# Performance work log

Hardware: AMD Instinct MI355X
Metric: run time of the kernel (lower is better)

Reference implementation:

```python
import jax, jax.numpy as jnp
import numpy as np

MARGIN = 200.0
EPS = 1e-6  # torch F.pairwise_distance default eps (added to the difference)


def setup_inputs() -> dict:
    key = jax.random.key(0)
    k1, k2, k3 = jax.random.split(key, 3)
    B2, T, D = 128, 1024, 1024  # 2*batch_size, snippets, feature dim
    scores = jax.random.normal(k1, (B2, T), dtype=jnp.float32)
    feats = jax.random.normal(k2, (B2, T, D), dtype=jnp.float32)
    targets = jax.random.uniform(k3, (B2, T), dtype=jnp.float32)
    return {"scores": scores, "feats": feats, "targets": targets}


def _bce_with_logits(logits, targets):
    # mean over all elements of max(x,0) - x*t + log(1+exp(-|x|))
    return jnp.mean(jnp.maximum(logits, 0.0) - logits * targets
                    + jnp.log1p(jnp.exp(-jnp.abs(logits))))


def _contrastive(M):
    # M: [2b, T] feature magnitudes (L1 norms). Split into normal / abnormal.
    b = M.shape[0] // 2
    n_f, a_f = M[:b], M[b:]
    # pairwise euclidean distance d_ij = ||n_i - a_j + eps||_2   [b, b]
    diff = n_f[:, None, :] - a_f[None, :, :] + EPS
    dist = jnp.sqrt(jnp.sum(diff * diff, axis=-1))
    d = jnp.square(jnp.maximum(MARGIN - dist, 0.0))
    # strict '<' in the torch loop => first flat occurrence of the min
    flat_idx = jnp.argmin(d.reshape(-1))
    i_star = flat_idx // b
    j_star = flat_idx % b
    min_d = d.reshape(-1)[flat_idx]
    loss_con = 0.001 * min_d
    # loss_n: sum_{i != i*} ||n_i - n_{i*} + eps||^2 / b
    dn = n_f - n_f[i_star] + EPS
    sq_n = jnp.sum(dn * dn, axis=-1)          # [b]
    loss_n = (jnp.sum(sq_n) - sq_n[i_star]) / b
    da = a_f - a_f[j_star] + EPS
    sq_a = jnp.sum(da * da, axis=-1)
    loss_a = (jnp.sum(sq_a) - sq_a[j_star]) / b
    return loss_con + loss_n + loss_a


def reference(scores, feats, targets):
    loss_cls = _bce_with_logits(scores, targets)
    mags = jnp.sum(jnp.abs(feats), axis=2)    # torch.norm(p=1, dim=2) -> [2b, T]
    loss_con = _contrastive(mags)
    return loss_cls + 0.001 * loss_con
```

## Files before the change

kernel.cpp:

```cpp
#include <hip/hip_runtime.h>
#include <math.h>

typedef float f32x4 __attribute__((ext_vector_type(4)));

#define NB2   128
#define NT    1024
#define ND    1024
#define BHALF 64
#define NROWS (NB2 * NT)
#define MARGIN_F 200.0f
#define EPS_F    1e-6f

#define MAGS_BLOCKS   2048
#define WAVES_TOTAL   (MAGS_BLOCKS*4)
#define ROWS_PER_WAVE (NROWS / WAVES_TOTAL)
#define BCE_BLOCKS    128


__device__ __forceinline__ float wave_reduce_sum(float s) {
#pragma unroll
    for (int off = 32; off > 0; off >>= 1)
        s += __shfl_xor(s, off, 64);
    return s;
}

__global__ void __launch_bounds__(256, 8)
main_kernel(const float* __restrict__ feats,
            const float* __restrict__ scores,
            const float* __restrict__ targets,
            float* __restrict__ mags,
            float* __restrict__ bce_part) {
    const int wave = threadIdx.x >> 6;
    const int lane = threadIdx.x & 63;

    if (blockIdx.x < BCE_BLOCKS) {
        const int idx = blockIdx.x * 256 + threadIdx.x;
        f32x4 l4 = reinterpret_cast<const f32x4*>(scores)[idx];
        f32x4 t4 = reinterpret_cast<const f32x4*>(targets)[idx];
        float s = 0.0f;
#pragma unroll
        for (int c = 0; c < 4; ++c) {
            float l = l4[c], t = t4[c];
            s += fmaxf(l, 0.0f) - l * t + log1pf(expf(-fabsf(l)));
        }
        s = wave_reduce_sum(s);
        __shared__ float lds[4];
        if (lane == 0) lds[wave] = s;
        __syncthreads();
        if (threadIdx.x == 0)
            bce_part[blockIdx.x] = lds[0] + lds[1] + lds[2] + lds[3];
    }

    const int gwave = blockIdx.x * 4 + wave;
    const float* base = feats + (size_t)gwave * ROWS_PER_WAVE * ND + lane * 4;
    float* mout = mags + (size_t)gwave * ROWS_PER_WAVE;

#pragma unroll 2
    for (int r = 0; r < ROWS_PER_WAVE; ++r) {
        const float* src = base + (size_t)r * ND;
        float s = 0.0f;
#pragma unroll
        for (int it = 0; it < 4; ++it) {
            f32x4 v = __builtin_nontemporal_load(
                reinterpret_cast<const f32x4*>(src + it * 256));
            s += fabsf(v.x) + fabsf(v.y) + fabsf(v.z) + fabsf(v.w);
        }
        s = wave_reduce_sum(s);
        if (lane == 0) mout[r] = s;
    }
}

__global__ void pairs_kernel(const float* __restrict__ mags,
                             float* __restrict__ dmat,
                             float* __restrict__ V) {
    __shared__ float p[4];
    const int wave = threadIdx.x >> 6;
    const int lane = threadIdx.x & 63;

    if (blockIdx.x < 1024) {
        const int pair = blockIdx.x * 4 + wave;
        const int i = pair >> 6;
        const int j = pair & 63;
        const float* nf = mags + (size_t)i * NT + lane * 4;
        const float* af = mags + (size_t)(BHALF + j) * NT + lane * 4;
        float s = 0.0f;
#pragma unroll
        for (int it = 0; it < 4; ++it) {
            f32x4 a = *reinterpret_cast<const f32x4*>(nf + it * 256);
            f32x4 b = *reinterpret_cast<const f32x4*>(af + it * 256);
#pragma unroll
            for (int c = 0; c < 4; ++c) {
                float dx = a[c] - b[c] + EPS_F;
                s += dx * dx;
            }
        }
        s = wave_reduce_sum(s);
        if (lane == 0) {
            float dist = sqrtf(s);
            float m = MARGIN_F - dist;
            dmat[pair] = (m > 0.0f) ? m * m : 0.0f;
        }
        return;
    }

    const int b    = blockIdx.x - 1024;
    const int half = b >> 6;
    const int i    = b & 63;
    const float* rowi = mags + (size_t)(half * BHALF + i) * NT + lane * 4;
    f32x4 ri[4];
#pragma unroll
    for (int it = 0; it < 4; ++it)
        ri[it] = *reinterpret_cast<const f32x4*>(rowi + it * 256);

    float s = 0.0f;
    for (int j = wave; j < BHALF; j += 4) {
        if (j == i) continue;
        const float* rowj = mags + (size_t)(half * BHALF + j) * NT + lane * 4;
#pragma unroll
        for (int it = 0; it < 4; ++it) {
            f32x4 vj = *reinterpret_cast<const f32x4*>(rowj + it * 256);
#pragma unroll
            for (int c = 0; c < 4; ++c) {
                float dx = vj[c] - ri[it][c] + EPS_F;
                s += dx * dx;
            }
        }
    }
    s = wave_reduce_sum(s);
    if (lane == 0) p[wave] = s;
    __syncthreads();
    if (threadIdx.x == 0)
        V[b] = p[0] + p[1] + p[2] + p[3];
}

__global__ void __launch_bounds__(1024)
mega_kernel(const float* __restrict__ dmat,
            const float* __restrict__ bce_part,
            const float* __restrict__ V,
            float* __restrict__ out) {
    __shared__ float sval[16];
    __shared__ int   sidx[16];
    __shared__ float bpart2[2];

    const int t    = threadIdx.x;
    const int wave = t >> 6;
    const int lane = t & 63;

    float best = INFINITY;
    int   bidx = 0x7FFFFFFF;
#pragma unroll
    for (int k = t; k < 4096; k += 1024) {
        float v = dmat[k];
        if (v < best || (v == best && k < bidx)) { best = v; bidx = k; }
    }
#pragma unroll
    for (int off = 32; off > 0; off >>= 1) {
        float v2 = __shfl_xor(best, off, 64);
        int   i2 = __shfl_xor(bidx, off, 64);
        if (v2 < best || (v2 == best && i2 < bidx)) { best = v2; bidx = i2; }
    }
    if (lane == 0) { sval[wave] = best; sidx[wave] = bidx; }

    if (t < 128) {
        float s = wave_reduce_sum(bce_part[t]);
        if (lane == 0) bpart2[wave] = s;
    }
    __syncthreads();

    if (t == 0) {
        float bv = sval[0]; int bi = sidx[0];
        for (int w = 1; w < 16; ++w)
            if (sval[w] < bv || (sval[w] == bv && sidx[w] < bi)) { bv = sval[w]; bi = sidx[w]; }
        const int istar = bi >> 6;
        const int jstar = bi & 63;
        float bce      = (bpart2[0] + bpart2[1]) / (float)NROWS;
        float loss_n   = V[istar] / (float)BHALF;
        float loss_a   = V[BHALF + jstar] / (float)BHALF;
        float contrast = 0.001f * bv + loss_n + loss_a;
        out[0] = bce + 0.001f * contrast;
    }
}

extern "C" void kernel_launch(void* const* d_in, const int* in_sizes, int n_in,
                              void* d_out, int out_size, void* d_ws, size_t ws_size,
                              hipStream_t stream) {
    const float* scores  = (const float*)d_in[0];
    const float* feats   = (const float*)d_in[1];
    const float* targets = (const float*)d_in[2];
    float* out      = (float*)d_out;
    float* ws       = (float*)d_ws;
    float* bce_part = ws + 64;
    float* V        = ws + 192;
    float* dmat     = ws + 1024;
    float* mags     = ws + 8192;

    main_kernel <<<MAGS_BLOCKS, 256, 0, stream>>>(feats, scores, targets, mags, bce_part);
    pairs_kernel<<<1024 + 128, 256, 0, stream>>>(mags, dmat, V);
    mega_kernel <<<1, 1024, 0, stream>>>(dmat, bce_part, V, out);
}
```

Measured before the change: 104.5 us.

## Fuse final reduction into pairs kernel via atomic counter; one row per wave

```diff
diff --git a/kernel.cpp b/kernel.cpp
--- a/kernel.cpp
+++ b/kernel.cpp
@@ -11,10 +11,11 @@
 #define MARGIN_F 200.0f
 #define EPS_F    1e-6f
 
-#define MAGS_BLOCKS   2048
-#define WAVES_TOTAL   (MAGS_BLOCKS*4)
-#define ROWS_PER_WAVE (NROWS / WAVES_TOTAL)
-#define BCE_BLOCKS    128
+#define MAGS_BLOCKS (NROWS / 4)
+#define BCE_BLOCKS  128
+#define PAIR_BLOCKS 1024
+#define V_BLOCKS    128
+#define TAIL_BLOCKS (PAIR_BLOCKS + V_BLOCKS)
 
 
 __device__ __forceinline__ float wave_reduce_sum(float s) {
@@ -24,60 +25,62 @@
     return s;
 }
 
-__global__ void __launch_bounds__(256, 8)
-main_kernel(const float* __restrict__ feats,
-            const float* __restrict__ scores,
-            const float* __restrict__ targets,
-            float* __restrict__ mags,
-            float* __restrict__ bce_part) {
+__global__ void main_kernel(const float* __restrict__ feats,
+                            const float* __restrict__ scores,
+                            const float* __restrict__ targets,
+                            float* __restrict__ mags,
+                            float* __restrict__ bce_part,
+                            int* __restrict__ counter) {
     const int wave = threadIdx.x >> 6;
     const int lane = threadIdx.x & 63;
 
-    if (blockIdx.x < BCE_BLOCKS) {
-        const int idx = blockIdx.x * 256 + threadIdx.x;
-        f32x4 l4 = reinterpret_cast<const f32x4*>(scores)[idx];
-        f32x4 t4 = reinterpret_cast<const f32x4*>(targets)[idx];
-        float s = 0.0f;
-#pragma unroll
-        for (int c = 0; c < 4; ++c) {
-            float l = l4[c], t = t4[c];
-            s += fmaxf(l, 0.0f) - l * t + log1pf(expf(-fabsf(l)));
-        }
-        s = wave_reduce_sum(s);
-        __shared__ float lds[4];
-        if (lane == 0) lds[wave] = s;
-        __syncthreads();
-        if (threadIdx.x == 0)
-            bce_part[blockIdx.x] = lds[0] + lds[1] + lds[2] + lds[3];
-    }
-
-    const int gwave = blockIdx.x * 4 + wave;
-    const float* base = feats + (size_t)gwave * ROWS_PER_WAVE * ND + lane * 4;
-    float* mout = mags + (size_t)gwave * ROWS_PER_WAVE;
-
-#pragma unroll 2
-    for (int r = 0; r < ROWS_PER_WAVE; ++r) {
-        const float* src = base + (size_t)r * ND;
+    if (blockIdx.x < MAGS_BLOCKS) {
+        const int row = blockIdx.x * 4 + wave;
+        const float* src = feats + (size_t)row * ND;
         float s = 0.0f;
 #pragma unroll
         for (int it = 0; it < 4; ++it) {
             f32x4 v = __builtin_nontemporal_load(
-                reinterpret_cast<const f32x4*>(src + it * 256));
+                reinterpret_cast<const f32x4*>(src + lane * 4 + it * 256));
             s += fabsf(v.x) + fabsf(v.y) + fabsf(v.z) + fabsf(v.w);
         }
         s = wave_reduce_sum(s);
-        if (lane == 0) mout[r] = s;
-    }
-}
-
-__global__ void pairs_kernel(const float* __restrict__ mags,
-                             float* __restrict__ dmat,
-                             float* __restrict__ V) {
+        if (lane == 0) mags[row] = s;
+        return;
+    }
+
+    const int b = blockIdx.x - MAGS_BLOCKS;
+    if (b == 0 && threadIdx.x == 0) *counter = 0;
+    const int idx = b * 256 + threadIdx.x;
+    f32x4 l4 = reinterpret_cast<const f32x4*>(scores)[idx];
+    f32x4 t4 = reinterpret_cast<const f32x4*>(targets)[idx];
+    float s = 0.0f;
+#pragma unroll
+    for (int c = 0; c < 4; ++c) {
+        float l = l4[c], t = t4[c];
+        s += fmaxf(l, 0.0f) - l * t + log1pf(expf(-fabsf(l)));
+    }
+    s = wave_reduce_sum(s);
+    __shared__ float lds[4];
+    if (lane == 0) lds[wave] = s;
+    __syncthreads();
+    if (threadIdx.x == 0)
+        bce_part[b] = lds[0] + lds[1] + lds[2] + lds[3];
+}
+
+__global__ void pairs_tail_kernel(const float* __restrict__ mags,
+                                  const float* __restrict__ bce_part,
+                                  float* __restrict__ dmat,
+                                  float* __restrict__ V,
+                                  int* __restrict__ counter,
+                                  float* __restrict__ out) {
     __shared__ float p[4];
+    __shared__ int   s_last;
     const int wave = threadIdx.x >> 6;
     const int lane = threadIdx.x & 63;
-
-    if (blockIdx.x < 1024) {
+    const int t    = threadIdx.x;
+
+    if (blockIdx.x < PAIR_BLOCKS) {
         const int pair = blockIdx.x * 4 + wave;
         const int i = pair >> 6;
         const int j = pair & 63;
@@ -99,57 +102,58 @@
             float dist = sqrtf(s);
             float m = MARGIN_F - dist;
             dmat[pair] = (m > 0.0f) ? m * m : 0.0f;
-        }
-        return;
-    }
-
-    const int b    = blockIdx.x - 1024;
-    const int half = b >> 6;
-    const int i    = b & 63;
-    const float* rowi = mags + (size_t)(half * BHALF + i) * NT + lane * 4;
-    f32x4 ri[4];
-#pragma unroll
-    for (int it = 0; it < 4; ++it)
-        ri[it] = *reinterpret_cast<const f32x4*>(rowi + it * 256);
-
-    float s = 0.0f;
-    for (int j = wave; j < BHALF; j += 4) {
-        if (j == i) continue;
-        const float* rowj = mags + (size_t)(half * BHALF + j) * NT + lane * 4;
-#pragma unroll
-        for (int it = 0; it < 4; ++it) {
-            f32x4 vj = *reinterpret_cast<const f32x4*>(rowj + it * 256);
-#pragma unroll
-            for (int c = 0; c < 4; ++c) {
-                float dx = vj[c] - ri[it][c] + EPS_F;
-                s += dx * dx;
+            __threadfence();
+        }
+    } else {
+        const int b    = blockIdx.x - PAIR_BLOCKS;
+        const int half = b >> 6;
+        const int i    = b & 63;
+        const float* rowi = mags + (size_t)(half * BHALF + i) * NT + lane * 4;
+        f32x4 ri[4];
+#pragma unroll
+        for (int it = 0; it < 4; ++it)
+            ri[it] = *reinterpret_cast<const f32x4*>(rowi + it * 256);
+
+        float s = 0.0f;
+        for (int j = wave; j < BHALF; j += 4) {
+            if (j == i) continue;
+            const float* rowj = mags + (size_t)(half * BHALF + j) * NT + lane * 4;
+#pragma unroll
+            for (int it = 0; it < 4; ++it) {
+                f32x4 vj = *reinterpret_cast<const f32x4*>(rowj + it * 256);
+#pragma unroll
+                for (int c = 0; c < 4; ++c) {
+                    float dx = vj[c] - ri[it][c] + EPS_F;
+                    s += dx * dx;
+                }
             }
         }
-    }
-    s = wave_reduce_sum(s);
-    if (lane == 0) p[wave] = s;
-    __syncthreads();
-    if (threadIdx.x == 0)
-        V[b] = p[0] + p[1] + p[2] + p[3];
-}
-
-__global__ void __launch_bounds__(1024)
-mega_kernel(const float* __restrict__ dmat,
-            const float* __restrict__ bce_part,
-            const float* __restrict__ V,
-            float* __restrict__ out) {
-    __shared__ float sval[16];
-    __shared__ int   sidx[16];
-    __shared__ float bpart2[2];
-
-    const int t    = threadIdx.x;
-    const int wave = t >> 6;
-    const int lane = t & 63;
+        s = wave_reduce_sum(s);
+        if (lane == 0) p[wave] = s;
+        __syncthreads();
+        if (t == 0) {
+            V[b] = p[0] + p[1] + p[2] + p[3];
+            __threadfence();
+        }
+    }
+
+    __syncthreads();
+    if (t == 0) {
+        int old = atomicAdd(counter, 1);
+        s_last = (old == TAIL_BLOCKS - 1) ? 1 : 0;
+    }
+    __syncthreads();
+    if (!s_last) return;
+
+    __threadfence();
+
+    __shared__ float sval[4];
+    __shared__ int   sidx[4];
+    __shared__ float bp[2];
 
     float best = INFINITY;
     int   bidx = 0x7FFFFFFF;
-#pragma unroll
-    for (int k = t; k < 4096; k += 1024) {
+    for (int k = t; k < 4096; k += 256) {
         float v = dmat[k];
         if (v < best || (v == best && k < bidx)) { best = v; bidx = k; }
     }
@@ -161,19 +165,20 @@
     }
     if (lane == 0) { sval[wave] = best; sidx[wave] = bidx; }
 
+    float bsum = 0.0f;
     if (t < 128) {
-        float s = wave_reduce_sum(bce_part[t]);
-        if (lane == 0) bpart2[wave] = s;
+        bsum = wave_reduce_sum(bce_part[t]);
+        if (lane == 0) bp[wave] = bsum;
     }
     __syncthreads();
 
     if (t == 0) {
         float bv = sval[0]; int bi = sidx[0];
-        for (int w = 1; w < 16; ++w)
+        for (int w = 1; w < 4; ++w)
             if (sval[w] < bv || (sval[w] == bv && sidx[w] < bi)) { bv = sval[w]; bi = sidx[w]; }
         const int istar = bi >> 6;
         const int jstar = bi & 63;
-        float bce      = (bpart2[0] + bpart2[1]) / (float)NROWS;
+        float bce      = (bp[0] + bp[1]) / (float)NROWS;
         float loss_n   = V[istar] / (float)BHALF;
         float loss_a   = V[BHALF + jstar] / (float)BHALF;
         float contrast = 0.001f * bv + loss_n + loss_a;
@@ -189,12 +194,14 @@
     const float* targets = (const float*)d_in[2];
     float* out      = (float*)d_out;
     float* ws       = (float*)d_ws;
+    int*   counter  = (int*)(ws + 32);
     float* bce_part = ws + 64;
     float* V        = ws + 192;
     float* dmat     = ws + 1024;
     float* mags     = ws + 8192;
 
-    main_kernel <<<MAGS_BLOCKS, 256, 0, stream>>>(feats, scores, targets, mags, bce_part);
-    pairs_kernel<<<1024 + 128, 256, 0, stream>>>(mags, dmat, V);
-    mega_kernel <<<1, 1024, 0, stream>>>(dmat, bce_part, V, out);
-}
+    main_kernel<<<MAGS_BLOCKS + BCE_BLOCKS, 256, 0, stream>>>(
+        feats, scores, targets, mags, bce_part, counter);
+    pairs_tail_kernel<<<TAIL_BLOCKS, 256, 0, stream>>>(
+        mags, bce_part, dmat, V, counter, out);
+}
```

Measured after the change: 164.6 us. 57.5% more time.
